# Performance work log

Measured on AMD Instinct MI355X. Metric: run time of the kernel, lower is better.

Reference implementation:

```python
import jax, jax.numpy as jnp
import numpy as np

B, N, K = 8, 2048, 100  # graphs per batch, nodes per graph, diffpool clusters


def _bn(x, g, b, eps=1e-5):
    # BatchNorm1d in training mode over all B*N nodes (biased variance)
    m = x.mean(axis=(0, 1))
    v = x.var(axis=(0, 1))
    return (x - m) * jax.lax.rsqrt(v + eps) * g + b


def _norm_adj(A):
    # PyG gcn_norm: add remaining self-loops (fill=1), D^-1/2 (A+I) D^-1/2
    n = A.shape[-1]
    d = jnp.diagonal(A, axis1=-2, axis2=-1)
    A_hat = A + jnp.where(d == 0, 1.0, 0.0)[..., :, None] * jnp.eye(n, dtype=A.dtype)
    deg = A_hat.sum(-1)
    dinv = jnp.where(deg > 0, 1.0 / jnp.sqrt(deg), 0.0)
    return dinv[..., :, None] * A_hat * dinv[..., None, :]


def _gcn(An, x, W, b):
    # GCNConv: propagate(x @ W) + bias, with pre-normalized adjacency
    return An @ (x @ W) + b


def _forward(x, adj, W_in, W3030, Wp13, b30, b100, Wfc_pool, bfc_pool,
             W1, b1, W2, b2, gamma30, beta30, gamma100, beta100):
    A_w = _norm_adj(adj)                               # weighted (edge_attr) adjacency
    A_b = _norm_adj((adj > 0).astype(adj.dtype))       # pool convs ignore edge_attr
    # feature branch
    x11 = _bn(_gcn(A_w, x, W_in[0], b30[0]), gamma30[0], beta30[0])
    x12 = _bn(_gcn(A_w, x11, W3030[0], b30[1]), gamma30[1], beta30[1])
    x13 = _bn(_gcn(A_w, x12, W3030[1], b30[2]), gamma30[2], beta30[2])
    x1_out = jnp.concatenate([x11, x12, x13], -1).max(axis=1)   # [B,90]
    # assignment branch
    s11 = _bn(_gcn(A_b, x, W_in[1], b30[3]), gamma30[3], beta30[3])
    s12 = _bn(_gcn(A_b, s11, W3030[2], b30[4]), gamma30[4], beta30[4])
    s13 = _bn(_gcn(A_b, s12, Wp13, b100), gamma100, beta100)
    s1 = jnp.concatenate([s11, s12, s13], -1) @ Wfc_pool + bfc_pool  # [B,N,K]
    # dense_diff_pool (link/entropy losses are unused by the forward output)
    s = jax.nn.softmax(s1, -1)
    p1_x = jnp.einsum('bnk,bnd->bkd', s, x13)          # s^T x  [B,K,30]
    p1_adj = jnp.einsum('bnk,bnl->bkl', s, adj @ s)    # s^T A s  [B,K,K]
    # second stage on pooled (dense, weighted) graph
    A2 = _norm_adj(p1_adj)
    x21 = _bn(_gcn(A2, p1_x, W3030[3], b30[5]), gamma30[5], beta30[5])
    x22 = _bn(_gcn(A2, x21, W3030[4], b30[6]), gamma30[6], beta30[6])
    x23 = _bn(_gcn(A2, x22, W3030[5], b30[7]), gamma30[7], beta30[7])
    x2_out = jnp.concatenate([x21, x22, x23], -1).max(axis=1)   # [B,90]
    h = jnp.concatenate([x1_out, x2_out], -1) @ W1 + b1
    return jax.nn.relu(h) @ W2 + b2                    # [B,6]


def setup_inputs():
    key = jax.random.key(0)
    ks = jax.random.split(key, 12)
    u = jax.random.uniform(ks[0], (B, N, N), dtype=jnp.float32)
    mask = jax.random.uniform(ks[1], (B, N, N)) < 0.05
    A = jnp.triu(u * mask, 1)
    adj = A + jnp.swapaxes(A, -1, -2)
    x = jax.random.normal(ks[2], (B, N, 3), dtype=jnp.float32)
    w = lambda k, s: jax.random.normal(k, s, dtype=jnp.float32) * 0.1
    return dict(
        x=x, adj=adj,
        W_in=w(ks[3], (2, 3, 30)),      # conv11, pool_conv11
        W3030=w(ks[4], (6, 30, 30)),    # conv12, conv13, pool_conv12, conv21..23
        Wp13=w(ks[5], (30, 100)),
        b30=jnp.zeros((8, 30), jnp.float32),
        b100=jnp.zeros((100,), jnp.float32),
        Wfc_pool=w(ks[6], (160, 100)), bfc_pool=jnp.zeros((100,), jnp.float32),
        W1=w(ks[7], (180, 50)), b1=jnp.zeros((50,), jnp.float32),
        W2=w(ks[8], (50, 6)), b2=jnp.zeros((6,), jnp.float32),
        gamma30=jnp.ones((8, 30), jnp.float32), beta30=jnp.zeros((8, 30), jnp.float32),
        gamma100=jnp.ones((100,), jnp.float32), beta100=jnp.zeros((100,), jnp.float32),
    )


def reference(x, adj, W_in, W3030, Wp13, b30, b100, Wfc_pool, bfc_pool,
              W1, b1, W2, b2, gamma30, beta30, gamma100, beta100):
    return _forward(x, adj, W_in, W3030, Wp13, b30, b100, Wfc_pool, bfc_pool,
                    W1, b1, W2, b2, gamma30, beta30, gamma100, beta100)
```

## Files before the change

### kernel.cpp

```cpp
#include <hip/hip_runtime.h>
#include <hip/hip_fp16.h>
#include <cstdint>
#include <cstddef>

#define BATCH 8
#define NN 2048
#define RTOT 16384

static constexpr size_t OF_B1W   = 0;
static constexpr size_t OF_B1B   = 3840;
static constexpr size_t OF_B2W   = 7680;
static constexpr size_t OF_B2B   = 11520;
static constexpr size_t OF_B3W   = 15360;
static constexpr size_t OF_B3B   = 15840;
static constexpr size_t OF_S2    = 17440;
static constexpr size_t OF_CNT   = 17620;
static constexpr size_t ZEND     = 17632;
static constexpr size_t OF_DINVW = 17664;
static constexpr size_t OF_DINVB = OF_DINVW + 16384;
static constexpr size_t OF_HWBT  = OF_DINVB + 16384;
static constexpr size_t OF_HW3T  = OF_HWBT + 524288;
static constexpr size_t OF_HBT   = OF_HW3T + 262144;
static constexpr size_t OF_ZW    = OF_HBT + 917504;
static constexpr size_t OF_ZB    = OF_ZW + 524288;
static constexpr size_t OF_X11   = OF_ZB + 1703936;
static constexpr size_t OF_X12   = OF_X11 + 524288;
static constexpr size_t OF_X13   = OF_X12 + 524288;
static constexpr size_t OF_S11   = OF_X13 + 524288;
static constexpr size_t OF_S12   = OF_S11 + 524288;
static constexpr size_t OF_PARTMAX = OF_S12 + 524288;
static constexpr size_t OF_PP    = OF_PARTMAX + 23040;
static constexpr size_t OF_PPOOL = OF_PP + 3328000;
static constexpr size_t OF_AW    = OF_PPOOL + 104000;
static constexpr size_t OF_AB    = OF_AW + 16777216;
static constexpr size_t OF_SROW  = OF_AB + 16777216;

typedef _Float16 f16x8 __attribute__((ext_vector_type(8)));
typedef float f32x4 __attribute__((ext_vector_type(4)));

#define FMA4(acc, s, h) { acc.x += (s)*(h).x; acc.y += (s)*(h).y; acc.z += (s)*(h).z; acc.w += (s)*(h).w; }

__device__ __forceinline__ unsigned short f2h(float f) {
  _Float16 h = (_Float16)f;
  return *(unsigned short*)&h;
}
__device__ __forceinline__ float h2f(unsigned short s) {
  _Float16 h = *(_Float16*)&s;
  return (float)h;
}

__device__ __forceinline__ size_t fidx(size_t blk, int lc, int k) {
  return ((blk * 64 + (k >> 5)) * 64 + ((k >> 3) & 3) * 16 + lc) * 8 + (k & 7);
}


__global__ __launch_bounds__(256) void k_build(
    const float* __restrict__ adj, const float* __restrict__ x,
    const float* __restrict__ Win,
    _Float16* __restrict__ Aw, _Float16* __restrict__ Ab,
    float* __restrict__ dinvw, float* __restrict__ dinvb,
    _Float16* __restrict__ HT, float* __restrict__ zbase)
{
  __shared__ float tile[16*516];
  __shared__ float dshw[16], dshb[16];
  int t = threadIdx.x;
  int blk = blockIdx.x;
  int r0 = blk << 4;
  size_t gph = (size_t)(r0 >> 11);
  if (blk < 69) {
    int zi = blk * 256 + t;
    if (zi < (int)ZEND) zbase[zi] = 0.f;
  }
  int lr = t >> 4, ls = t & 15;
  const float* rowp = adj + (size_t)(r0 + lr) * NN;
  float sum = 0.f; int cnt = 0;
  for (int ch = 0; ch < 4; ++ch) {
    int c0 = ch << 9;
    __syncthreads();
    const float4* rp = (const float4*)(rowp + c0);
#pragma unroll
    for (int i = 0; i < 8; ++i) {
      float4 v = rp[ls + (i << 4)];
      sum += v.x + v.y + v.z + v.w;
      cnt += (v.x != 0.f) + (v.y != 0.f) + (v.z != 0.f) + (v.w != 0.f);
      *(float4*)&tile[lr*516 + ls*4 + (i << 6)] = v;
    }
    __syncthreads();
    int kbG = (ch << 4) + lr;
    size_t base = (((size_t)blk * 4096) + (size_t)kbG * 64 + (size_t)ls * 4) * 8;
#pragma unroll
    for (int j = 0; j < 4; ++j) {
      int u = ls*4 + j;
      int kg = u >> 4, lc = u & 15;
      int crel = lr*32 + kg*8;
      const float* src = &tile[lc*516 + crel];
      int R = r0 + lc;
      int cg0 = c0 + crel;
      f16x8 wv, bv;
#pragma unroll
      for (int e = 0; e < 8; ++e) {
        float v = src[e];
        bool dg = (cg0 + e) == R;
        wv[e] = (_Float16)(dg ? 1.f : v);
        bv[e] = (_Float16)((dg || v != 0.f) ? 1.f : 0.f);
      }
      *(f16x8*)(Aw + base + j*8) = wv;
      *(f16x8*)(Ab + base + j*8) = bv;
    }
  }
#pragma unroll
  for (int o = 8; o; o >>= 1) { sum += __shfl_down(sum, o); cnt += __shfl_down(cnt, o); }
  if (ls == 0) {
    int R = r0 + lr;
    float dw = rsqrtf(sum + 1.f), db = rsqrtf((float)cnt + 1.f);
    dinvw[R] = dw; dinvb[R] = db;
    dshw[lr] = dw; dshb[lr] = db;
  }
  __syncthreads();
  {
    int R = r0 + lr, rloc = R & (NN-1);
    float x0 = x[R*3], x1 = x[R*3+1], x2 = x[R*3+2];
#pragma unroll
    for (int e = 0; e < 4; ++e) {
      int c = ls*4 + e;
      int side = c >> 5, cc = c & 31;
      float v = 0.f;
      if (cc < 30) {
        const float* W = Win + side*90;
        v = (x0*W[cc] + x1*W[30+cc] + x2*W[60+cc]) * (side ? dshb[lr] : dshw[lr]);
      }
      HT[fidx(gph*4 + (c >> 4), c & 15, rloc)] = (_Float16)v;
    }
  }
}

__global__ __launch_bounds__(256, 2) void k_gemm_pair(
    const _Float16* __restrict__ Aw, const _Float16* __restrict__ Ab,
    const _Float16* __restrict__ HT,
    const float* __restrict__ dinvw, const float* __restrict__ dinvb,
    float* __restrict__ Zw, float* __restrict__ Zb,
    float* __restrict__ bktW, float* __restrict__ bktB)
{
  __shared__ float zs[64][32];
  int t = threadIdx.x;
  int side = blockIdx.x >> 8;
  int mb = blockIdx.x & 255;
  int row0 = mb << 6;
  size_t g = (size_t)(row0 >> 11);
  int w = t >> 6, l = t & 63, lc = l & 15, kg = l >> 4;
  const _Float16* A = side ? Ab : Aw;
  size_t rowblk = g*128 + ((row0 & 2047) >> 4) + w;
  const _Float16* Af  = A  + (rowblk * 64) * 512 + l * 8;
  const _Float16* Bf0 = HT + ((g*4 + side*2) * 64) * 512 + l * 8;
  const _Float16* Bf1 = Bf0 + (size_t)64 * 512;
  f32x4 acc0 = {0,0,0,0}, acc1 = {0,0,0,0};
#pragma unroll 8
  for (int kb = 0; kb < 64; ++kb) {
    f16x8 af = *(const f16x8*)(Af  + kb*512);
    f16x8 b0 = *(const f16x8*)(Bf0 + kb*512);
    f16x8 b1 = *(const f16x8*)(Bf1 + kb*512);
    acc0 = __builtin_amdgcn_mfma_f32_16x16x32_f16(af, b0, acc0, 0, 0, 0);
    acc1 = __builtin_amdgcn_mfma_f32_16x16x32_f16(af, b1, acc1, 0, 0, 0);
  }
  int rb = (w << 4) + (kg << 2);
#pragma unroll
  for (int i = 0; i < 4; ++i) { zs[rb + i][lc] = acc0[i]; zs[rb + i][16 + lc] = acc1[i]; }
  __syncthreads();
  {
    int r = t >> 2, c8 = (t & 3) << 3;
    float d = (side ? dinvb : dinvw)[row0 + r];
    float o[8];
#pragma unroll
    for (int j = 0; j < 8; ++j) o[j] = zs[r][c8 + j] * d;
#pragma unroll
    for (int j = 0; j < 8; ++j) zs[r][c8 + j] = o[j];
    float* Zp = (side ? Zb : Zw) + (((size_t)(row0 + r)) << 5) + c8;
    float4 o0 = {o[0],o[1],o[2],o[3]}, o1 = {o[4],o[5],o[6],o[7]};
    ((float4*)Zp)[0] = o0; ((float4*)Zp)[1] = o1;
  }
  __syncthreads();
  int copy = blockIdx.x & 63;
  if (t < 30) {
    float s1 = 0.f, s2 = 0.f;
    for (int r = 0; r < 64; ++r) { float v = zs[r][t]; s1 += v; s2 += v*v; }
    float* bkt = side ? bktB : bktW;
    atomicAdd(&bkt[(t*64+copy)*2],   s1);
    atomicAdd(&bkt[(t*64+copy)*2+1], s2);
  }
}

__global__ __launch_bounds__(256, 2) void k_gemm_l3(
    const _Float16* __restrict__ Aw, const _Float16* __restrict__ Ab,
    const _Float16* __restrict__ Hw3T, const _Float16* __restrict__ HbT,
    const float* __restrict__ dinvw, const float* __restrict__ dinvb,
    float* __restrict__ Zw, float* __restrict__ Zb,
    float* __restrict__ bktW3, float* __restrict__ bktB3)
{
  __shared__ float zsst[2048];
  int t = threadIdx.x;
  int w = t >> 6, l = t & 63, lc = l & 15, kg = l >> 4;
  if (blockIdx.x < 256) {
    int row0 = blockIdx.x << 6;
    size_t g = (size_t)(row0 >> 11);
    size_t rowblk = g*128 + ((row0 & 2047) >> 4) + w;
    const _Float16* Af  = Aw   + (rowblk * 64) * 512 + l * 8;
    const _Float16* Bf0 = Hw3T + ((g*2) * 64) * 512 + l * 8;
    const _Float16* Bf1 = Bf0 + (size_t)64 * 512;
    f32x4 acc0 = {0,0,0,0}, acc1 = {0,0,0,0};
#pragma unroll 8
    for (int kb = 0; kb < 64; ++kb) {
      f16x8 af = *(const f16x8*)(Af  + kb*512);
      f16x8 b0 = *(const f16x8*)(Bf0 + kb*512);
      f16x8 b1 = *(const f16x8*)(Bf1 + kb*512);
      acc0 = __builtin_amdgcn_mfma_f32_16x16x32_f16(af, b0, acc0, 0, 0, 0);
      acc1 = __builtin_amdgcn_mfma_f32_16x16x32_f16(af, b1, acc1, 0, 0, 0);
    }
    float (*zs)[32] = (float (*)[32])zsst;
    int rb = (w << 4) + (kg << 2);
#pragma unroll
    for (int i = 0; i < 4; ++i) { zs[rb + i][lc] = acc0[i]; zs[rb + i][16 + lc] = acc1[i]; }
    __syncthreads();
    {
      int r = t >> 2, c8 = (t & 3) << 3;
      float d = dinvw[row0 + r];
      float o[8];
#pragma unroll
      for (int j = 0; j < 8; ++j) o[j] = zs[r][c8 + j] * d;
#pragma unroll
      for (int j = 0; j < 8; ++j) zs[r][c8 + j] = o[j];
      float* Zp = Zw + (((size_t)(row0 + r)) << 5) + c8;
      float4 o0 = {o[0],o[1],o[2],o[3]}, o1 = {o[4],o[5],o[6],o[7]};
      ((float4*)Zp)[0] = o0; ((float4*)Zp)[1] = o1;
    }
    __syncthreads();
    if (t < 30) {
      float s1 = 0.f, s2 = 0.f;
      for (int r = 0; r < 64; ++r) { float v = zs[r][t]; s1 += v; s2 += v*v; }
      int copy = blockIdx.x & 7;
      atomicAdd(&bktW3[(t*8+copy)*2],   s1);
      atomicAdd(&bktW3[(t*8+copy)*2+1], s2);
    }
  } else {
    int row0 = (blockIdx.x - 256) << 6;
    size_t g = (size_t)(row0 >> 11);
    size_t rowblk = g*128 + ((row0 & 2047) >> 4) + w;
    const _Float16* Af = Ab + (rowblk * 64) * 512 + l * 8;
    for (int s = t; s < 200; s += 256) zsst[s] = 0.f;
    const _Float16* Bf = HbT + ((g*7) * 64) * 512 + l * 8;
    f32x4 acc[7];
#pragma unroll
    for (int f = 0; f < 7; ++f) acc[f] = (f32x4){0,0,0,0};
#pragma unroll 4
    for (int kb = 0; kb < 64; ++kb) {
      f16x8 af = *(const f16x8*)(Af + kb*512);
#pragma unroll
      for (int f = 0; f < 7; ++f) {
        f16x8 bf = *(const f16x8*)(Bf + (size_t)f*32768 + kb*512);
        acc[f] = __builtin_amdgcn_mfma_f32_16x16x32_f16(af, bf, acc[f], 0, 0, 0);
      }
    }
    __syncthreads();
    int rb = (w << 4) + (kg << 2);
    float d[4];
#pragma unroll
    for (int i = 0; i < 4; ++i) d[i] = dinvb[row0 + rb + i];
#pragma unroll
    for (int f = 0; f < 7; ++f) {
      int col = f*16 + lc;
#pragma unroll
      for (int i = 0; i < 4; ++i) {
        float v = acc[f][i] * d[i];
        if (col < 104) Zb[(size_t)(row0 + rb + i) * 104 + col] = v;
        if (col < 100) { atomicAdd(&zsst[col*2], v); atomicAdd(&zsst[col*2+1], v*v); }
      }
    }
    __syncthreads();
    int copy = blockIdx.x & 7;
    for (int i2 = t; i2 < 200; i2 += 256)
      atomicAdd(&bktB3[((i2>>1)*8 + copy)*2 + (i2&1)], zsst[i2]);
  }
}

__global__ __launch_bounds__(256, 2) void k_gemm_as(
    const _Float16* __restrict__ Aw, const _Float16* __restrict__ ST,
    const unsigned short* __restrict__ Srow, float* __restrict__ As)
{
  int t = threadIdx.x;
  int w = t >> 6, l = t & 63, lc = l & 15, kg = l >> 4;
  int row0 = blockIdx.x << 6;
  size_t g = (size_t)(row0 >> 11);
  size_t rowblk = g*128 + ((row0 & 2047) >> 4) + w;
  const _Float16* Af = Aw + (rowblk * 64) * 512 + l * 8;
  const _Float16* Bf = ST + ((g*7) * 64) * 512 + l * 8;
  f32x4 acc[7];
#pragma unroll
  for (int f = 0; f < 7; ++f) acc[f] = (f32x4){0,0,0,0};
#pragma unroll 4
  for (int kb = 0; kb < 64; ++kb) {
    f16x8 af = *(const f16x8*)(Af + kb*512);
#pragma unroll
    for (int f = 0; f < 7; ++f) {
      f16x8 bf = *(const f16x8*)(Bf + (size_t)f*32768 + kb*512);
      acc[f] = __builtin_amdgcn_mfma_f32_16x16x32_f16(af, bf, acc[f], 0, 0, 0);
    }
  }
  int rb = (w << 4) + (kg << 2);
#pragma unroll
  for (int f = 0; f < 7; ++f) {
    int col = f*16 + lc;
#pragma unroll
    for (int i = 0; i < 4; ++i) {
      int row = row0 + rb + i;
      if (col < 104)
        As[(size_t)row * 104 + col] = acc[f][i] - h2f(Srow[(size_t)row * 104 + col]);
    }
  }
}

template<int LEVEL>
__global__ __launch_bounds__(256) void k_apply_gemm(
    const float* __restrict__ Zw, const float* __restrict__ bktW,
    const float* __restrict__ gW, const float* __restrict__ beW,
    float* __restrict__ xst, const float* __restrict__ Ww,
    const float* __restrict__ dinvw,
    const float* __restrict__ Zb, const float* __restrict__ bktB,
    const float* __restrict__ gB, const float* __restrict__ beB,
    float* __restrict__ sst, const float* __restrict__ Wb,
    const float* __restrict__ dinvb,
    _Float16* __restrict__ HwOutT, _Float16* __restrict__ HbOutT)
{
  constexpr int NGB = (LEVEL == 1) ? 8 : 26;
  constexpr int OSTRIDEB = (LEVEL == 1) ? 32 : 104;
  constexpr int NG = 8 + NGB;
  __shared__ float WwL[30*32];
  __shared__ float WbL[30*OSTRIDEB];
  __shared__ float awL[60], abL[60];
  int t = threadIdx.x;
  if (t < 60) {
    int c = t % 30;
    bool isW = t < 30;
    const float4* p = (const float4*)((isW ? bktW : bktB) + c*128);
    float s1 = 0.f, s2 = 0.f;
#pragma unroll
    for (int k = 0; k < 32; ++k) { float4 v = p[k]; s1 += v.x + v.z; s2 += v.y + v.w; }
    float mean = s1/16384.f, var = s2/16384.f - mean*mean, inv = rsqrtf(var + 1e-5f);
    float aa = (isW ? gW : gB)[c]*inv;
    float* dst = isW ? awL : abL;
    dst[c] = aa; dst[30+c] = (isW ? beW : beB)[c] - mean*aa;
  }
  for (int idx = t; idx < 30*32; idx += 256) {
    int k = idx >> 5, c = idx & 31;
    WwL[idx] = (c < 30) ? Ww[k*30 + c] : 0.f;
  }
  if (LEVEL == 1) {
    for (int idx = t; idx < 30*32; idx += 256) {
      int k = idx >> 5, c = idx & 31;
      WbL[idx] = (c < 30) ? Wb[k*30 + c] : 0.f;
    }
  } else {
    for (int idx = t; idx < 30*OSTRIDEB; idx += 256) {
      int k = idx / OSTRIDEB, j = idx % OSTRIDEB;
      WbL[idx] = (j < 100) ? Wb[k*100 + j] : 0.f;
    }
  }
  __syncthreads();
  int gid = blockIdx.x * 256 + t;
  int row = gid / NG, g = gid % NG;
  size_t gph = (size_t)(row >> 11);
  int rloc = row & (NN-1);
  if (g < 8) {
    const float4* Z4 = (const float4*)Zw + (size_t)row*8;
    float4 z4[8];
#pragma unroll
    for (int u = 0; u < 8; ++u) z4[u] = Z4[u];
    const float* z = (const float*)z4;
    int ch = 4*g;
    float4 zg = Z4[g];
    float4 xv;
    xv.x = (ch+0 < 30) ? awL[ch+0]*zg.x + awL[30+ch+0] : 0.f;
    xv.y = (ch+1 < 30) ? awL[ch+1]*zg.y + awL[30+ch+1] : 0.f;
    xv.z = (ch+2 < 30) ? awL[ch+2]*zg.z + awL[30+ch+2] : 0.f;
    xv.w = (ch+3 < 30) ? awL[ch+3]*zg.w + awL[30+ch+3] : 0.f;
    ((float4*)xst)[(size_t)row*8+g] = xv;
    float4 o = {0,0,0,0};
#pragma unroll
    for (int k = 0; k < 30; ++k) {
      float xk = awL[k]*z[k] + awL[30+k];
      float4 w = *(const float4*)(WwL + k*32 + 4*g);
      FMA4(o, xk, w);
    }
    float d = dinvw[row];
    float ov[4] = {d*o.x, d*o.y, d*o.z, d*o.w};
#pragma unroll
    for (int i = 0; i < 4; ++i) {
      int col = ch + i;
      if (LEVEL == 1) HwOutT[fidx(gph*4 + (col>>4), col & 15, rloc)] = (_Float16)ov[i];
      else            HwOutT[fidx(gph*2 + (col>>4), col & 15, rloc)] = (_Float16)ov[i];
    }
  } else {
    int gb = g - 8;
    const float4* Z4 = (const float4*)Zb + (size_t)row*8;
    float4 z4[8];
#pragma unroll
    for (int u = 0; u < 8; ++u) z4[u] = Z4[u];
    const float* z = (const float*)z4;
    if (gb < 8) {
      int ch = 4*gb;
      float4 zg = Z4[gb];
      float4 sv;
      sv.x = (ch+0 < 30) ? abL[ch+0]*zg.x + abL[30+ch+0] : 0.f;
      sv.y = (ch+1 < 30) ? abL[ch+1]*zg.y + abL[30+ch+1] : 0.f;
      sv.z = (ch+2 < 30) ? abL[ch+2]*zg.z + abL[30+ch+2] : 0.f;
      sv.w = (ch+3 < 30) ? abL[ch+3]*zg.w + abL[30+ch+3] : 0.f;
      ((float4*)sst)[(size_t)row*8+gb] = sv;
    }
    float4 o = {0,0,0,0};
#pragma unroll
    for (int k = 0; k < 30; ++k) {
      float sk = abL[k]*z[k] + abL[30+k];
      float4 w = *(const float4*)(WbL + k*OSTRIDEB + 4*gb);
      FMA4(o, sk, w);
    }
    float d = dinvb[row];
    float ov[4] = {d*o.x, d*o.y, d*o.z, d*o.w};
#pragma unroll
    for (int i = 0; i < 4; ++i) {
      int col = 4*gb + i;
      if (LEVEL == 1) { int c2 = 32 + col; HbOutT[fidx(gph*4 + (c2>>4), c2 & 15, rloc)] = (_Float16)ov[i]; }
      else            HbOutT[fidx(gph*7 + (col>>4), col & 15, rloc)] = (_Float16)ov[i];
    }
    if (LEVEL == 2) {
      if (gb == 24) {
#pragma unroll
        for (int c = 104; c < 108; ++c) HbOutT[fidx(gph*7 + 6, c & 15, rloc)] = (_Float16)0.f;
      } else if (gb == 25) {
#pragma unroll
        for (int c = 108; c < 112; ++c) HbOutT[fidx(gph*7 + 6, c & 15, rloc)] = (_Float16)0.f;
      }
    }
  }
}

__global__ __launch_bounds__(256) void k_fcpool(
    const float* __restrict__ Zw3, const float* __restrict__ bktW3,
    const float* __restrict__ gW3, const float* __restrict__ beW3,
    const float* __restrict__ Zb3, const float* __restrict__ bktB3,
    const float* __restrict__ g100, const float* __restrict__ be100,
    const float* __restrict__ s11, const float* __restrict__ s12,
    const float* __restrict__ Wfc, const float* __restrict__ bfc,
    float* __restrict__ x13, unsigned short* __restrict__ Srow,
    _Float16* __restrict__ ST)
{
  __shared__ float shm[14240];
  __shared__ float aw3[60], ab3[200];
  float* feat = shm;
  float* Wl = shm + 10240;
  int t = threadIdx.x;
  int g0 = blockIdx.x * 64;
  size_t gph = (size_t)(g0 >> 11);
  if (t < 30) {
    const float4* p = (const float4*)(bktW3 + t*16);
    float s1 = 0.f, s2 = 0.f;
#pragma unroll
    for (int k = 0; k < 4; ++k) { float4 v = p[k]; s1 += v.x + v.z; s2 += v.y + v.w; }
    float mean = s1/16384.f, var = s2/16384.f - mean*mean, inv = rsqrtf(var + 1e-5f);
    float aa = gW3[t]*inv; aw3[t] = aa; aw3[30+t] = beW3[t] - mean*aa;
  } else if (t >= 64 && t < 164) {
    int c = t - 64;
    const float4* p = (const float4*)(bktB3 + c*16);
    float s1 = 0.f, s2 = 0.f;
#pragma unroll
    for (int k = 0; k < 4; ++k) { float4 v = p[k]; s1 += v.x + v.z; s2 += v.y + v.w; }
    float mean = s1/16384.f, var = s2/16384.f - mean*mean, inv = rsqrtf(var + 1e-5f);
    float aa = g100[c]*inv; ab3[c] = aa; ab3[100+c] = be100[c] - mean*aa;
  }
  __syncthreads();
  for (int idx = t; idx < 64*160; idx += 256) {
    int l = idx / 160, c = idx % 160;
    int g = g0 + l;
    float v;
    if (c < 30) v = s11[(size_t)g*32 + c];
    else if (c < 60) v = s12[(size_t)g*32 + (c-30)];
    else { int k = c - 60; v = ab3[k]*Zb3[(size_t)g*104 + k] + ab3[100 + k]; }
    feat[l*160 + c] = v;
  }
  for (int idx = t; idx < 64*32; idx += 256) {
    int l = idx >> 5, c = idx & 31;
    int g = g0 + l;
    x13[(size_t)g*32+c] = (c < 30) ? aw3[c]*Zw3[(size_t)g*32+c] + aw3[30+c] : 0.f;
  }
  int np = t >> 3, kg = t & 7;
  int n0 = np*2, n1 = np*2 + 1;
  int kbase = kg*12 + (kg < 4 ? kg : 4);
  int klen  = kg < 4 ? 13 : 12;
  float a0[13], a1[13];
#pragma unroll
  for (int j = 0; j < 13; ++j) { a0[j] = 0.f; a1[j] = 0.f; }
  for (int ch = 0; ch < 4; ++ch) {
    __syncthreads();
    for (int idx = t; idx < 4000; idx += 256) {
      int r = idx/100, j = idx%100;
      Wl[r*100 + j] = Wfc[(ch*40 + r)*100 + j];
    }
    __syncthreads();
    for (int kk = 0; kk < 40; ++kk) {
      float f0 = feat[n0*160 + ch*40+kk];
      float f1 = feat[n1*160 + ch*40+kk];
#pragma unroll
      for (int j = 0; j < 13; ++j) {
        if (j < klen) {
          float w = Wl[kk*100 + kbase + j];
          a0[j] += f0*w; a1[j] += f1*w;
        }
      }
    }
  }
  __syncthreads();
  float* sRow = shm;
  for (int j = 0; j < klen; ++j) {
    int k = kbase + j;
    sRow[n0*100 + k] = a0[j] + bfc[k];
    sRow[n1*100 + k] = a1[j] + bfc[k];
  }
  __syncthreads();
  int n = t >> 2, part = t & 3;
  int i0 = part*25;
  int rloc = (g0 + n) & (NN-1);
  float m = -3.4e38f;
  for (int i = 0; i < 25; ++i) m = fmaxf(m, sRow[n*100 + i0 + i]);
  m = fmaxf(m, __shfl_xor(m, 1));
  m = fmaxf(m, __shfl_xor(m, 2));
  float ev[25]; float s = 0.f;
  for (int i = 0; i < 25; ++i) { float e = __expf(sRow[n*100 + i0 + i] - m); ev[i] = e; s += e; }
  s += __shfl_xor(s, 1);
  s += __shfl_xor(s, 2);
  float rinv = 1.f / s;
  for (int i = 0; i < 25; ++i) {
    float v = ev[i] * rinv;
    int c = i0 + i;
    Srow[(size_t)(g0+n)*104 + c] = f2h(v);
    ST[fidx(gph*7 + (c>>4), c & 15, rloc)] = (_Float16)v;
  }
  if (part == 3) {
#pragma unroll
    for (int c = 100; c < 104; ++c) Srow[(size_t)(g0+n)*104 + c] = 0;
#pragma unroll
    for (int c = 100; c < 112; ++c) ST[fidx(gph*7 + (c>>4), c & 15, rloc)] = (_Float16)0.f;
  }
}

__global__ __launch_bounds__(256) void k_pool_part(
    const unsigned short* __restrict__ S, const float* __restrict__ x13,
    const float* __restrict__ As, const float* __restrict__ x11,
    const float* __restrict__ x12, float* __restrict__ pp, float* __restrict__ pm)
{
  __shared__ float sL[64][100];
  __shared__ float xL[64][132];
  __shared__ float red[256];
  int t = threadIdx.x;
  int b = blockIdx.x >> 5, chunk = blockIdx.x & 31;
  int g0 = b * 2048 + chunk * 64;
  int kt = t/10, dt = t%10;
  int k0 = kt*4, d0 = dt*13;
  float acc[4][13];
#pragma unroll
  for (int a = 0; a < 4; ++a)
#pragma unroll
    for (int j = 0; j < 13; ++j) acc[a][j] = 0.f;
  for (int idx = t; idx < 64*100; idx += 256) {
    int l = idx/100, k = idx%100;
    sL[l][k] = h2f(S[(size_t)(g0+l)*104 + k]);
  }
  for (int idx = t; idx < 64*130; idx += 256) {
    int l = idx/130, d = idx%130;
    xL[l][d] = d < 30 ? x13[(size_t)(g0+l)*32 + d] : As[(size_t)(g0+l)*104 + (d-30)];
  }
  __syncthreads();
  if (t < 250) {
    for (int kk = 0; kk < 64; ++kk) {
      float sv[4];
#pragma unroll
      for (int a = 0; a < 4; ++a) sv[a] = sL[kk][k0+a];
#pragma unroll
      for (int j = 0; j < 13; ++j) {
        float xv = xL[kk][d0+j];
#pragma unroll
        for (int a = 0; a < 4; ++a) acc[a][j] += sv[a]*xv;
      }
    }
    float* dst = pp + (size_t)blockIdx.x * 13000;
    for (int a = 0; a < 4; ++a)
      for (int j = 0; j < 13; ++j)
        dst[(k0+a)*130 + (d0+j)] = acc[a][j];
  }
  __syncthreads();
  {
    int c = t & 31, rg = t >> 5;
    const float* srcs[3] = {x11, x12, x13};
#pragma unroll
    for (int a = 0; a < 3; ++a) {
      const float* p = srcs[a] + (size_t)(g0+rg)*32 + c;
      float m = -3.4e38f;
#pragma unroll
      for (int it = 0; it < 8; ++it) m = fmaxf(m, p[it*256]);
      red[t] = m;
      __syncthreads();
      if (t < 30) {
        float mm = red[t];
        for (int g = 1; g < 8; ++g) mm = fmaxf(mm, red[g*32+t]);
        pm[(size_t)blockIdx.x*90 + a*30 + t] = mm;
      }
      __syncthreads();
    }
  }
}

__global__ __launch_bounds__(256) void k_pool_reduce(
    const float* __restrict__ pp, float* __restrict__ ppool)
{
  int b = blockIdx.x / 51, blk = blockIdx.x % 51;
  int idx = blk * 256 + threadIdx.x;
  if (idx < 13000) {
    const float* src = pp + (size_t)b * 32 * 13000 + idx;
    float s = 0.f;
#pragma unroll
    for (int c = 0; c < 32; ++c) s += src[c*13000];
    ppool[(size_t)b*13000 + idx] = s;
  }
}

__global__ __launch_bounds__(256) void k_s2fused(
    const float* __restrict__ ppool, const float* __restrict__ partmax,
    const float* __restrict__ Wm,
    const float* __restrict__ g30,
    const float* __restrict__ be30,
    float* __restrict__ bktS2,
    int* __restrict__ cnt,
    const float* __restrict__ W1, const float* __restrict__ b1,
    const float* __restrict__ W2, const float* __restrict__ b2,
    float* __restrict__ out)
{
  __shared__ float A2f[10000];
  __shared__ float buf1[3000];
  __shared__ float buf2[3200];
  __shared__ float WL[960];
  __shared__ float dl[100];
  __shared__ float st1[30], st2[30];
  __shared__ float coef[60];
  __shared__ float x1L[90], x2L[90], hh[50];
  int b = blockIdx.x, t = threadIdx.x;
  for (int idx = t; idx < 13000; idx += 256) {
    float s = ppool[(size_t)b*13000 + idx];
    int k = idx/130, d = idx%130;
    if (d < 30) buf1[k*30 + d] = s;
    else A2f[k*100 + (d-30)] = s;
  }
  __syncthreads();
  if (t < 100 && A2f[t*101] == 0.f) A2f[t*101] = 1.f;
  __syncthreads();
  if (t < 100) {
    float s = 0.f;
    for (int j = 0; j < 100; ++j) s += A2f[t*100 + j];
    dl[t] = s > 0.f ? rsqrtf(s) : 0.f;
  }
  __syncthreads();
  for (int idx = t; idx < 10000; idx += 256) {
    int i = idx/100, j = idx%100;
    A2f[idx] = dl[i]*dl[j]*A2f[idx];
  }
  int rp = t >> 2, cg = t & 3;
  int i0 = rp*2, c0 = cg*8;
  bool act = (t < 200);
  for (int L = 0; L < 3; ++L) {
    if (t < 30) { st1[t] = 0.f; st2[t] = 0.f; }
    const float* W = Wm + L*900;
    for (int idx = t; idx < 960; idx += 256) {
      int k = idx >> 5, c = idx & 31;
      WL[idx] = (c < 30) ? W[k*30 + c] : 0.f;
    }
    __syncthreads();
    if (act) {
      float a0[8] = {0,0,0,0,0,0,0,0}, a1[8] = {0,0,0,0,0,0,0,0};
      for (int k = 0; k < 30; ++k) {
        float xx0 = buf1[i0*30 + k], xx1 = buf1[(i0+1)*30 + k];
        float4 w0 = *(const float4*)&WL[k*32 + c0];
        float4 w1 = *(const float4*)&WL[k*32 + c0 + 4];
        a0[0] += xx0*w0.x; a0[1] += xx0*w0.y; a0[2] += xx0*w0.z; a0[3] += xx0*w0.w;
        a0[4] += xx0*w1.x; a0[5] += xx0*w1.y; a0[6] += xx0*w1.z; a0[7] += xx0*w1.w;
        a1[0] += xx1*w0.x; a1[1] += xx1*w0.y; a1[2] += xx1*w0.z; a1[3] += xx1*w0.w;
        a1[4] += xx1*w1.x; a1[5] += xx1*w1.y; a1[6] += xx1*w1.z; a1[7] += xx1*w1.w;
      }
      float4 s00 = {a0[0],a0[1],a0[2],a0[3]}, s01 = {a0[4],a0[5],a0[6],a0[7]};
      float4 s10 = {a1[0],a1[1],a1[2],a1[3]}, s11v = {a1[4],a1[5],a1[6],a1[7]};
      *(float4*)&buf2[i0*32 + c0]       = s00;
      *(float4*)&buf2[i0*32 + c0 + 4]   = s01;
      *(float4*)&buf2[(i0+1)*32 + c0]   = s10;
      *(float4*)&buf2[(i0+1)*32 + c0+4] = s11v;
    }
    __syncthreads();
    if (act) {
      float z0[8] = {0,0,0,0,0,0,0,0}, z1[8] = {0,0,0,0,0,0,0,0};
      for (int j = 0; j < 100; ++j) {
        float av0 = A2f[i0*100 + j], av1 = A2f[(i0+1)*100 + j];
        float4 t0 = *(const float4*)&buf2[j*32 + c0];
        float4 t1 = *(const float4*)&buf2[j*32 + c0 + 4];
        z0[0] += av0*t0.x; z0[1] += av0*t0.y; z0[2] += av0*t0.z; z0[3] += av0*t0.w;
        z0[4] += av0*t1.x; z0[5] += av0*t1.y; z0[6] += av0*t1.z; z0[7] += av0*t1.w;
        z1[0] += av1*t0.x; z1[1] += av1*t0.y; z1[2] += av1*t0.z; z1[3] += av1*t0.w;
        z1[4] += av1*t1.x; z1[5] += av1*t1.y; z1[6] += av1*t1.z; z1[7] += av1*t1.w;
      }
#pragma unroll
      for (int k = 0; k < 8; ++k) {
        int c = c0 + k;
        if (c < 30) {
          buf1[i0*30 + c]     = z0[k];
          buf1[(i0+1)*30 + c] = z1[k];
          atomicAdd(&st1[c], z0[k] + z1[k]);
          atomicAdd(&st2[c], z0[k]*z0[k] + z1[k]*z1[k]);
        }
      }
    }
    __syncthreads();
    if (t < 30) {
      atomicAdd(&bktS2[(L*30+t)*2],   st1[t]);
      atomicAdd(&bktS2[(L*30+t)*2+1], st2[t]);
    }
    __syncthreads();
    if (t == 0) {
      __threadfence();
      atomicAdd(cnt, 1);
      while (atomicAdd(cnt, 0) < (L+1)*8) {}
      __threadfence();
    }
    __syncthreads();
    if (t < 30) {
      float s1 = atomicAdd(&bktS2[(L*30+t)*2],   0.f);
      float s2 = atomicAdd(&bktS2[(L*30+t)*2+1], 0.f);
      float mean = s1/800.f, var = s2/800.f - mean*mean, inv = rsqrtf(var + 1e-5f);
      float aa = g30[L*30+t]*inv;
      coef[t] = aa; coef[30+t] = be30[L*30+t] - mean*aa;
    }
    __syncthreads();
    if (L < 2) {
      for (int idx = t; idx < 3000; idx += 256) {
        int c = idx % 30;
        buf1[idx] = coef[c]*buf1[idx] + coef[30+c];
      }
      __syncthreads();
      if (t < 30) {
        float m = -3.4e38f;
        for (int i = 0; i < 100; ++i) m = fmaxf(m, buf1[i*30+t]);
        x2L[L*30+t] = m;
      }
      __syncthreads();
    } else {
      if (t < 30) {
        float m = -3.4e38f;
        for (int i = 0; i < 100; ++i) m = fmaxf(m, coef[t]*buf1[i*30+t] + coef[30+t]);
        x2L[60+t] = m;
      }
    }
  }
  if (t < 90) {
    float m = -3.4e38f;
    for (int s = 0; s < 32; ++s) m = fmaxf(m, partmax[(size_t)(b*32+s)*90 + t]);
    x1L[t] = m;
  }
  __syncthreads();
  if (t < 50) {
    float a = b1[t];
    for (int k = 0; k < 90; ++k) a += x1L[k]*W1[k*50+t];
    for (int k = 0; k < 90; ++k) a += x2L[k]*W1[(90+k)*50+t];
    hh[t] = fmaxf(a, 0.f);
  }
  __syncthreads();
  if (t < 6) {
    float a = b2[t];
    for (int j = 0; j < 50; ++j) a += hh[j]*W2[j*6+t];
    out[b*6+t] = a;
  }
}

extern "C" void kernel_launch(void* const* d_in, const int* in_sizes, int n_in,
                              void* d_out, int out_size, void* d_ws, size_t ws_size,
                              hipStream_t stream)
{
  const float* x    = (const float*)d_in[0];
  const float* adj  = (const float*)d_in[1];
  const float* Win  = (const float*)d_in[2];
  const float* W3030= (const float*)d_in[3];
  const float* Wp13 = (const float*)d_in[4];
  const float* Wfc  = (const float*)d_in[7];
  const float* bfc  = (const float*)d_in[8];
  const float* W1   = (const float*)d_in[9];
  const float* b1   = (const float*)d_in[10];
  const float* W2   = (const float*)d_in[11];
  const float* b2   = (const float*)d_in[12];
  const float* g30  = (const float*)d_in[13];
  const float* be30 = (const float*)d_in[14];
  const float* g100 = (const float*)d_in[15];
  const float* be100= (const float*)d_in[16];
  float* out = (float*)d_out;

  float* wsf = (float*)d_ws;
  float* bL1W = wsf + OF_B1W;  float* bL1B = wsf + OF_B1B;
  float* bL2W = wsf + OF_B2W;  float* bL2B = wsf + OF_B2B;
  float* bL3W = wsf + OF_B3W;  float* bL3B = wsf + OF_B3B;
  float* bktS2 = wsf + OF_S2;
  int*   cnt  = (int*)(wsf + OF_CNT);
  float* dinvw = wsf + OF_DINVW;
  float* dinvb = wsf + OF_DINVB;
  _Float16* HwbT = (_Float16*)(wsf + OF_HWBT);
  _Float16* Hw3T = (_Float16*)(wsf + OF_HW3T);
  _Float16* HbT  = (_Float16*)(wsf + OF_HBT);
  float* Zw = wsf + OF_ZW;
  float* Zb = wsf + OF_ZB;
  float* x11 = wsf + OF_X11;
  float* x12 = wsf + OF_X12;
  float* x13 = wsf + OF_X13;
  float* s11 = wsf + OF_S11;
  float* s12 = wsf + OF_S12;
  float* pp  = wsf + OF_PP;
  float* ppool = wsf + OF_PPOOL;
  float* partmax = wsf + OF_PARTMAX;
  _Float16* Aw = (_Float16*)(wsf + OF_AW);
  _Float16* Ab = (_Float16*)(wsf + OF_AB);
  unsigned short* Srow = (unsigned short*)(wsf + OF_SROW);

  k_build<<<1024, 256, 0, stream>>>(adj, x, Win, Aw, Ab, dinvw, dinvb, HwbT, wsf);

  k_gemm_pair<<<512, 256, 0, stream>>>(Aw, Ab, HwbT, dinvw, dinvb, Zw, Zb, bL1W, bL1B);
  k_apply_gemm<1><<<1024, 256, 0, stream>>>(Zw, bL1W, g30+0, be30+0, x11, W3030+0, dinvw,
                                            Zb, bL1B, g30+90, be30+90, s11, W3030+2*900, dinvb, HwbT, HwbT);

  k_gemm_pair<<<512, 256, 0, stream>>>(Aw, Ab, HwbT, dinvw, dinvb, Zw, Zb, bL2W, bL2B);
  k_apply_gemm<2><<<2176, 256, 0, stream>>>(Zw, bL2W, g30+30, be30+30, x12, W3030+900, dinvw,
                                            Zb, bL2B, g30+120, be30+120, s12, Wp13, dinvb, Hw3T, HbT);

  k_gemm_l3<<<512, 256, 0, stream>>>(Aw, Ab, Hw3T, HbT, dinvw, dinvb, Zw, Zb, bL3W, bL3B);
  k_fcpool<<<256, 256, 0, stream>>>(Zw, bL3W, g30+60, be30+60, Zb, bL3B, g100, be100,
                                    s11, s12, Wfc, bfc, x13, Srow, HbT );

  k_gemm_as<<<256, 256, 0, stream>>>(Aw, HbT , Srow, Zb );
  k_pool_part<<<256, 256, 0, stream>>>(Srow, x13, Zb, x11, x12, pp, partmax);
  k_pool_reduce<<<408, 256, 0, stream>>>(pp, ppool);

  k_s2fused<<<BATCH, 256, 0, stream>>>(ppool, partmax, W3030+3*900, g30+150, be30+150,
                                       bktS2, cnt, W1, b1, W2, b2, out);
}
```

Baseline: 611.6 us.

## Halve GEMM row tiles and split output columns across waves for more blocks

The MFMA propagation kernels (pair, l3, as) now use 32-row blocks instead of 64. The four waves split as two row halves by two column groups, and the launch grids double. The aim is more blocks and waves in flight to hide global-load latency on the memory-bound A·H GEMMs, with launch bounds raised to 3 blocks per CU. In exchange, each A row-block is loaded twice per block (once per column-group wave), adding redundant A traffic, and the batch-norm statistics take twice as many atomics.

After: 641.5 us. +4.9%, slower.

```diff
diff --git a/kernel.cpp b/kernel.cpp
--- a/kernel.cpp
+++ b/kernel.cpp
@@ -134,183 +134,199 @@
   }
 }
 
-__global__ __launch_bounds__(256, 2) void k_gemm_pair(
+__global__ __launch_bounds__(256, 3) void k_gemm_pair(
     const _Float16* __restrict__ Aw, const _Float16* __restrict__ Ab,
     const _Float16* __restrict__ HT,
     const float* __restrict__ dinvw, const float* __restrict__ dinvb,
     float* __restrict__ Zw, float* __restrict__ Zb,
     float* __restrict__ bktW, float* __restrict__ bktB)
 {
-  __shared__ float zs[64][32];
+  __shared__ float zs[32][32];
   int t = threadIdx.x;
-  int side = blockIdx.x >> 8;
-  int mb = blockIdx.x & 255;
-  int row0 = mb << 6;
+  int side = blockIdx.x >> 9;
+  int rg = blockIdx.x & 511;
+  int row0 = rg << 5;
   size_t g = (size_t)(row0 >> 11);
   int w = t >> 6, l = t & 63, lc = l & 15, kg = l >> 4;
+  int rowhalf = w & 1, colhalf = w >> 1;
   const _Float16* A = side ? Ab : Aw;
-  size_t rowblk = g*128 + ((row0 & 2047) >> 4) + w;
-  const _Float16* Af  = A  + (rowblk * 64) * 512 + l * 8;
-  const _Float16* Bf0 = HT + ((g*4 + side*2) * 64) * 512 + l * 8;
-  const _Float16* Bf1 = Bf0 + (size_t)64 * 512;
-  f32x4 acc0 = {0,0,0,0}, acc1 = {0,0,0,0};
-#pragma unroll 8
+  size_t rowblk = g*128 + ((row0 & 2047) >> 4) + rowhalf;
+  const _Float16* Af = A  + (rowblk * 64) * 512 + l * 8;
+  const _Float16* Bf = HT + (((size_t)(g*4 + side*2 + colhalf)) * 64) * 512 + l * 8;
+  f32x4 acc = {0,0,0,0};
+#pragma unroll 16
   for (int kb = 0; kb < 64; ++kb) {
-    f16x8 af = *(const f16x8*)(Af  + kb*512);
-    f16x8 b0 = *(const f16x8*)(Bf0 + kb*512);
-    f16x8 b1 = *(const f16x8*)(Bf1 + kb*512);
-    acc0 = __builtin_amdgcn_mfma_f32_16x16x32_f16(af, b0, acc0, 0, 0, 0);
-    acc1 = __builtin_amdgcn_mfma_f32_16x16x32_f16(af, b1, acc1, 0, 0, 0);
-  }
-  int rb = (w << 4) + (kg << 2);
-#pragma unroll
-  for (int i = 0; i < 4; ++i) { zs[rb + i][lc] = acc0[i]; zs[rb + i][16 + lc] = acc1[i]; }
+    f16x8 af = *(const f16x8*)(Af + kb*512);
+    f16x8 bf = *(const f16x8*)(Bf + kb*512);
+    acc = __builtin_amdgcn_mfma_f32_16x16x32_f16(af, bf, acc, 0, 0, 0);
+  }
+#pragma unroll
+  for (int i = 0; i < 4; ++i) zs[rowhalf*16 + kg*4 + i][colhalf*16 + lc] = acc[i];
   __syncthreads();
   {
-    int r = t >> 2, c8 = (t & 3) << 3;
+    int r = t >> 3, c4 = (t & 7) << 2;
     float d = (side ? dinvb : dinvw)[row0 + r];
-    float o[8];
-#pragma unroll
-    for (int j = 0; j < 8; ++j) o[j] = zs[r][c8 + j] * d;
-#pragma unroll
-    for (int j = 0; j < 8; ++j) zs[r][c8 + j] = o[j];
-    float* Zp = (side ? Zb : Zw) + (((size_t)(row0 + r)) << 5) + c8;
-    float4 o0 = {o[0],o[1],o[2],o[3]}, o1 = {o[4],o[5],o[6],o[7]};
-    ((float4*)Zp)[0] = o0; ((float4*)Zp)[1] = o1;
+    float4 o;
+    o.x = zs[r][c4+0] * d; o.y = zs[r][c4+1] * d;
+    o.z = zs[r][c4+2] * d; o.w = zs[r][c4+3] * d;
+    zs[r][c4+0] = o.x; zs[r][c4+1] = o.y; zs[r][c4+2] = o.z; zs[r][c4+3] = o.w;
+    float* Zp = (side ? Zb : Zw) + (((size_t)(row0 + r)) << 5) + c4;
+    *(float4*)Zp = o;
   }
   __syncthreads();
   int copy = blockIdx.x & 63;
   if (t < 30) {
     float s1 = 0.f, s2 = 0.f;
-    for (int r = 0; r < 64; ++r) { float v = zs[r][t]; s1 += v; s2 += v*v; }
+    for (int r = 0; r < 32; ++r) { float v = zs[r][t]; s1 += v; s2 += v*v; }
     float* bkt = side ? bktB : bktW;
     atomicAdd(&bkt[(t*64+copy)*2],   s1);
     atomicAdd(&bkt[(t*64+copy)*2+1], s2);
   }
 }
 
-__global__ __launch_bounds__(256, 2) void k_gemm_l3(
+__global__ __launch_bounds__(256, 3) void k_gemm_l3(
     const _Float16* __restrict__ Aw, const _Float16* __restrict__ Ab,
     const _Float16* __restrict__ Hw3T, const _Float16* __restrict__ HbT,
     const float* __restrict__ dinvw, const float* __restrict__ dinvb,
     float* __restrict__ Zw, float* __restrict__ Zb,
     float* __restrict__ bktW3, float* __restrict__ bktB3)
 {
-  __shared__ float zsst[2048];
+  __shared__ float zsst[1024];
   int t = threadIdx.x;
   int w = t >> 6, l = t & 63, lc = l & 15, kg = l >> 4;
-  if (blockIdx.x < 256) {
-    int row0 = blockIdx.x << 6;
+  if (blockIdx.x < 512) {
+    int row0 = blockIdx.x << 5;
     size_t g = (size_t)(row0 >> 11);
-    size_t rowblk = g*128 + ((row0 & 2047) >> 4) + w;
-    const _Float16* Af  = Aw   + (rowblk * 64) * 512 + l * 8;
-    const _Float16* Bf0 = Hw3T + ((g*2) * 64) * 512 + l * 8;
-    const _Float16* Bf1 = Bf0 + (size_t)64 * 512;
-    f32x4 acc0 = {0,0,0,0}, acc1 = {0,0,0,0};
-#pragma unroll 8
+    int rowhalf = w & 1, colhalf = w >> 1;
+    size_t rowblk = g*128 + ((row0 & 2047) >> 4) + rowhalf;
+    const _Float16* Af = Aw   + (rowblk * 64) * 512 + l * 8;
+    const _Float16* Bf = Hw3T + (((size_t)(g*2 + colhalf)) * 64) * 512 + l * 8;
+    f32x4 acc = {0,0,0,0};
+#pragma unroll 16
     for (int kb = 0; kb < 64; ++kb) {
-      f16x8 af = *(const f16x8*)(Af  + kb*512);
-      f16x8 b0 = *(const f16x8*)(Bf0 + kb*512);
-      f16x8 b1 = *(const f16x8*)(Bf1 + kb*512);
-      acc0 = __builtin_amdgcn_mfma_f32_16x16x32_f16(af, b0, acc0, 0, 0, 0);
-      acc1 = __builtin_amdgcn_mfma_f32_16x16x32_f16(af, b1, acc1, 0, 0, 0);
+      f16x8 af = *(const f16x8*)(Af + kb*512);
+      f16x8 bf = *(const f16x8*)(Bf + kb*512);
+      acc = __builtin_amdgcn_mfma_f32_16x16x32_f16(af, bf, acc, 0, 0, 0);
     }
     float (*zs)[32] = (float (*)[32])zsst;
-    int rb = (w << 4) + (kg << 2);
-#pragma unroll
-    for (int i = 0; i < 4; ++i) { zs[rb + i][lc] = acc0[i]; zs[rb + i][16 + lc] = acc1[i]; }
+#pragma unroll
+    for (int i = 0; i < 4; ++i) zs[rowhalf*16 + kg*4 + i][colhalf*16 + lc] = acc[i];
     __syncthreads();
     {
-      int r = t >> 2, c8 = (t & 3) << 3;
+      int r = t >> 3, c4 = (t & 7) << 2;
       float d = dinvw[row0 + r];
-      float o[8];
-#pragma unroll
-      for (int j = 0; j < 8; ++j) o[j] = zs[r][c8 + j] * d;
-#pragma unroll
-      for (int j = 0; j < 8; ++j) zs[r][c8 + j] = o[j];
-      float* Zp = Zw + (((size_t)(row0 + r)) << 5) + c8;
-      float4 o0 = {o[0],o[1],o[2],o[3]}, o1 = {o[4],o[5],o[6],o[7]};
-      ((float4*)Zp)[0] = o0; ((float4*)Zp)[1] = o1;
+      float4 o;
+      o.x = zs[r][c4+0] * d; o.y = zs[r][c4+1] * d;
+      o.z = zs[r][c4+2] * d; o.w = zs[r][c4+3] * d;
+      zs[r][c4+0] = o.x; zs[r][c4+1] = o.y; zs[r][c4+2] = o.z; zs[r][c4+3] = o.w;
+      float* Zp = Zw + (((size_t)(row0 + r)) << 5) + c4;
+      *(float4*)Zp = o;
     }
     __syncthreads();
     if (t < 30) {
       float s1 = 0.f, s2 = 0.f;
-      for (int r = 0; r < 64; ++r) { float v = zs[r][t]; s1 += v; s2 += v*v; }
+      for (int r = 0; r < 32; ++r) { float v = zs[r][t]; s1 += v; s2 += v*v; }
       int copy = blockIdx.x & 7;
       atomicAdd(&bktW3[(t*8+copy)*2],   s1);
       atomicAdd(&bktW3[(t*8+copy)*2+1], s2);
     }
   } else {
-    int row0 = (blockIdx.x - 256) << 6;
+    int bid = blockIdx.x - 512;
+    int row0 = bid << 5;
     size_t g = (size_t)(row0 >> 11);
-    size_t rowblk = g*128 + ((row0 & 2047) >> 4) + w;
+    int rowhalf = w & 1, fgrp = w >> 1;
+    size_t rowblk = g*128 + ((row0 & 2047) >> 4) + rowhalf;
     const _Float16* Af = Ab + (rowblk * 64) * 512 + l * 8;
     for (int s = t; s < 200; s += 256) zsst[s] = 0.f;
-    const _Float16* Bf = HbT + ((g*7) * 64) * 512 + l * 8;
-    f32x4 acc[7];
-#pragma unroll
-    for (int f = 0; f < 7; ++f) acc[f] = (f32x4){0,0,0,0};
-#pragma unroll 4
+    int f0 = fgrp * 4, nf = fgrp ? 3 : 4;
+    const _Float16* Bf = HbT + (((size_t)(g*7 + f0)) * 64) * 512 + l * 8;
+    f32x4 acc[4];
+#pragma unroll
+    for (int f = 0; f < 4; ++f) acc[f] = (f32x4){0,0,0,0};
+    if (nf == 4) {
+#pragma unroll 8
+      for (int kb = 0; kb < 64; ++kb) {
+        f16x8 af = *(const f16x8*)(Af + kb*512);
+#pragma unroll
+        for (int f = 0; f < 4; ++f) {
+          f16x8 bf = *(const f16x8*)(Bf + (size_t)f*32768 + kb*512);
+          acc[f] = __builtin_amdgcn_mfma_f32_16x16x32_f16(af, bf, acc[f], 0, 0, 0);
+        }
+      }
+    } else {
+#pragma unroll 8
+      for (int kb = 0; kb < 64; ++kb) {
+        f16x8 af = *(const f16x8*)(Af + kb*512);
+#pragma unroll
+        for (int f = 0; f < 3; ++f) {
+          f16x8 bf = *(const f16x8*)(Bf + (size_t)f*32768 + kb*512);
+          acc[f] = __builtin_amdgcn_mfma_f32_16x16x32_f16(af, bf, acc[f], 0, 0, 0);
+        }
+      }
+    }
+    __syncthreads();
+    float d[4];
+#pragma unroll
+    for (int i = 0; i < 4; ++i) d[i] = dinvb[row0 + rowhalf*16 + kg*4 + i];
+    for (int f = 0; f < nf; ++f) {
+      int col = (f0 + f)*16 + lc;
+#pragma unroll
+      for (int i = 0; i < 4; ++i) {
+        float v = acc[f][i] * d[i];
+        int row = row0 + rowhalf*16 + kg*4 + i;
+        if (col < 104) Zb[(size_t)row * 104 + col] = v;
+        if (col < 100) { atomicAdd(&zsst[col*2], v); atomicAdd(&zsst[col*2+1], v*v); }
+      }
+    }
+    __syncthreads();
+    int copy = bid & 7;
+    for (int i2 = t; i2 < 200; i2 += 256)
+      atomicAdd(&bktB3[((i2>>1)*8 + copy)*2 + (i2&1)], zsst[i2]);
+  }
+}
+
+__global__ __launch_bounds__(256, 3) void k_gemm_as(
+    const _Float16* __restrict__ Aw, const _Float16* __restrict__ ST,
+    const unsigned short* __restrict__ Srow, float* __restrict__ As)
+{
+  int t = threadIdx.x;
+  int w = t >> 6, l = t & 63, lc = l & 15, kg = l >> 4;
+  int row0 = blockIdx.x << 5;
+  size_t g = (size_t)(row0 >> 11);
+  int rowhalf = w & 1, fgrp = w >> 1;
+  size_t rowblk = g*128 + ((row0 & 2047) >> 4) + rowhalf;
+  const _Float16* Af = Aw + (rowblk * 64) * 512 + l * 8;
+  int f0 = fgrp * 4, nf = fgrp ? 3 : 4;
+  const _Float16* Bf = ST + (((size_t)(g*7 + f0)) * 64) * 512 + l * 8;
+  f32x4 acc[4];
+#pragma unroll
+  for (int f = 0; f < 4; ++f) acc[f] = (f32x4){0,0,0,0};
+  if (nf == 4) {
+#pragma unroll 8
     for (int kb = 0; kb < 64; ++kb) {
       f16x8 af = *(const f16x8*)(Af + kb*512);
 #pragma unroll
-      for (int f = 0; f < 7; ++f) {
+      for (int f = 0; f < 4; ++f) {
         f16x8 bf = *(const f16x8*)(Bf + (size_t)f*32768 + kb*512);
         acc[f] = __builtin_amdgcn_mfma_f32_16x16x32_f16(af, bf, acc[f], 0, 0, 0);
       }
     }
-    __syncthreads();
-    int rb = (w << 4) + (kg << 2);
-    float d[4];
-#pragma unroll
-    for (int i = 0; i < 4; ++i) d[i] = dinvb[row0 + rb + i];
-#pragma unroll
-    for (int f = 0; f < 7; ++f) {
-      int col = f*16 + lc;
-#pragma unroll
-      for (int i = 0; i < 4; ++i) {
-        float v = acc[f][i] * d[i];
-        if (col < 104) Zb[(size_t)(row0 + rb + i) * 104 + col] = v;
-        if (col < 100) { atomicAdd(&zsst[col*2], v); atomicAdd(&zsst[col*2+1], v*v); }
-      }
-    }
-    __syncthreads();
-    int copy = blockIdx.x & 7;
-    for (int i2 = t; i2 < 200; i2 += 256)
-      atomicAdd(&bktB3[((i2>>1)*8 + copy)*2 + (i2&1)], zsst[i2]);
-  }
-}
-
-__global__ __launch_bounds__(256, 2) void k_gemm_as(
-    const _Float16* __restrict__ Aw, const _Float16* __restrict__ ST,
-    const unsigned short* __restrict__ Srow, float* __restrict__ As)
-{
-  int t = threadIdx.x;
-  int w = t >> 6, l = t & 63, lc = l & 15, kg = l >> 4;
-  int row0 = blockIdx.x << 6;
-  size_t g = (size_t)(row0 >> 11);
-  size_t rowblk = g*128 + ((row0 & 2047) >> 4) + w;
-  const _Float16* Af = Aw + (rowblk * 64) * 512 + l * 8;
-  const _Float16* Bf = ST + ((g*7) * 64) * 512 + l * 8;
-  f32x4 acc[7];
-#pragma unroll
-  for (int f = 0; f < 7; ++f) acc[f] = (f32x4){0,0,0,0};
-#pragma unroll 4
-  for (int kb = 0; kb < 64; ++kb) {
-    f16x8 af = *(const f16x8*)(Af + kb*512);
-#pragma unroll
-    for (int f = 0; f < 7; ++f) {
-      f16x8 bf = *(const f16x8*)(Bf + (size_t)f*32768 + kb*512);
-      acc[f] = __builtin_amdgcn_mfma_f32_16x16x32_f16(af, bf, acc[f], 0, 0, 0);
-    }
-  }
-  int rb = (w << 4) + (kg << 2);
-#pragma unroll
-  for (int f = 0; f < 7; ++f) {
-    int col = f*16 + lc;
+  } else {
+#pragma unroll 8
+    for (int kb = 0; kb < 64; ++kb) {
+      f16x8 af = *(const f16x8*)(Af + kb*512);
+#pragma unroll
+      for (int f = 0; f < 3; ++f) {
+        f16x8 bf = *(const f16x8*)(Bf + (size_t)f*32768 + kb*512);
+        acc[f] = __builtin_amdgcn_mfma_f32_16x16x32_f16(af, bf, acc[f], 0, 0, 0);
+      }
+    }
+  }
+  for (int f = 0; f < nf; ++f) {
+    int col = (f0 + f)*16 + lc;
 #pragma unroll
     for (int i = 0; i < 4; ++i) {
-      int row = row0 + rb + i;
+      int row = row0 + rowhalf*16 + kg*4 + i;
       if (col < 104)
         As[(size_t)row * 104 + col] = acc[f][i] - h2f(Srow[(size_t)row * 104 + col]);
     }
@@ -829,19 +845,19 @@
 
   k_build<<<1024, 256, 0, stream>>>(adj, x, Win, Aw, Ab, dinvw, dinvb, HwbT, wsf);
 
-  k_gemm_pair<<<512, 256, 0, stream>>>(Aw, Ab, HwbT, dinvw, dinvb, Zw, Zb, bL1W, bL1B);
+  k_gemm_pair<<<1024, 256, 0, stream>>>(Aw, Ab, HwbT, dinvw, dinvb, Zw, Zb, bL1W, bL1B);
   k_apply_gemm<1><<<1024, 256, 0, stream>>>(Zw, bL1W, g30+0, be30+0, x11, W3030+0, dinvw,
                                             Zb, bL1B, g30+90, be30+90, s11, W3030+2*900, dinvb, HwbT, HwbT);
 
-  k_gemm_pair<<<512, 256, 0, stream>>>(Aw, Ab, HwbT, dinvw, dinvb, Zw, Zb, bL2W, bL2B);
+  k_gemm_pair<<<1024, 256, 0, stream>>>(Aw, Ab, HwbT, dinvw, dinvb, Zw, Zb, bL2W, bL2B);
   k_apply_gemm<2><<<2176, 256, 0, stream>>>(Zw, bL2W, g30+30, be30+30, x12, W3030+900, dinvw,
                                             Zb, bL2B, g30+120, be30+120, s12, Wp13, dinvb, Hw3T, HbT);
 
-  k_gemm_l3<<<512, 256, 0, stream>>>(Aw, Ab, Hw3T, HbT, dinvw, dinvb, Zw, Zb, bL3W, bL3B);
+  k_gemm_l3<<<1024, 256, 0, stream>>>(Aw, Ab, Hw3T, HbT, dinvw, dinvb, Zw, Zb, bL3W, bL3B);
   k_fcpool<<<256, 256, 0, stream>>>(Zw, bL3W, g30+60, be30+60, Zb, bL3B, g100, be100,
                                     s11, s12, Wfc, bfc, x13, Srow, HbT );
 
-  k_gemm_as<<<256, 256, 0, stream>>>(Aw, HbT , Srow, Zb );
+  k_gemm_as<<<512, 256, 0, stream>>>(Aw, HbT , Srow, Zb );
   k_pool_part<<<256, 256, 0, stream>>>(Srow, x13, Zb, x11, x12, pp, partmax);
   k_pool_reduce<<<408, 256, 0, stream>>>(pp, ppool);
 
```
